# Performance work log

Hardware: AMD Instinct MI355X
Metric: run time of the kernel (lower is better)

The kernel has to match this reference:

```python
import jax, jax.numpy as jnp
import numpy as np

B, T, D = 4, 256, 512          # batch, seq_len, encoder_dim
L, H = 2, 8                    # num xLSTM blocks, num heads
I = 2 * D                      # inner dim (proj_factor=2)
DH = I // H                    # per-head dim = 128
K, G = 32, 64                  # mdn_components, goal_dim
EPS = 1e-5


def _ln(x, s, b):
    m = x.mean(-1, keepdims=True)
    v = jnp.mean((x - m) ** 2, -1, keepdims=True)
    return (x - m) * jax.lax.rsqrt(v + EPS) * s + b


def setup_inputs() -> dict:
    key = jax.random.key(0)
    ks = jax.random.split(key, 16)
    sc = 0.02
    nrm = lambda k, shp: jax.random.normal(k, shp, jnp.float32) * sc
    return {
        "x": jax.random.normal(ks[0], (B, T, D), jnp.float32),
        "ln_s": jnp.ones((L, D), jnp.float32),
        "ln_b": jnp.zeros((L, D), jnp.float32),
        "W_proj": nrm(ks[1], (L, D, 2 * I)),
        "Wq": nrm(ks[2], (L, I, I)),
        "Wk": nrm(ks[3], (L, I, I)),
        "Wv": nrm(ks[4], (L, I, I)),
        "Wi": nrm(ks[5], (L, I, H)),
        "bi": jnp.zeros((L, H), jnp.float32),
        "Wf": nrm(ks[6], (L, I, H)),
        "bf": jnp.full((L, H), 3.0, jnp.float32),  # forget-gate bias init
        "gn_s": jnp.ones((L, I), jnp.float32),
        "gn_b": jnp.zeros((L, I), jnp.float32),
        "W_down": nrm(ks[7], (L, I, D)),
        "fln_s": jnp.ones((D,), jnp.float32),
        "fln_b": jnp.zeros((D,), jnp.float32),
        "W_pi": nrm(ks[8], (D, K)),
        "b_pi": jnp.zeros((K,), jnp.float32),
        "W_mu": nrm(ks[9], (D, K * G)),
        "b_mu": jnp.zeros((K * G,), jnp.float32),
        "W_sig": nrm(ks[10], (D, K * G)),
        "b_sig": jnp.zeros((K * G,), jnp.float32),
    }


def _forward(x, ln_s, ln_b, W_proj, Wq, Wk, Wv, Wi, bi, Wf, bf,
             gn_s, gn_b, W_down, fln_s, fln_b,
             W_pi, b_pi, W_mu, b_mu, W_sig, b_sig):
    inv_sqrt_dh = 1.0 / (DH ** 0.5)

    def step(carry, x_t):  # x_t: (B, D); replicates per-timestep xlstm_stack.step()
        C, n, m = carry    # (L,B,H,DH,DH), (L,B,H,DH), (L,B,H)
        h = x_t
        for l in range(L):  # fixed small block loop
            skip = h
            xn = _ln(h, ln_s[l], ln_b[l])
            xp = xn @ W_proj[l]                      # (B, 2I)
            xm, z = jnp.split(xp, 2, axis=-1)        # mLSTM branch / gate branch
            q = (xm @ Wq[l]).reshape(B, H, DH)
            k = (xm @ Wk[l]).reshape(B, H, DH) * inv_sqrt_dh
            v = (xm @ Wv[l]).reshape(B, H, DH)
            ip = xm @ Wi[l] + bi[l]                  # (B, H) exp input gate preact
            fp = xm @ Wf[l] + bf[l]                  # (B, H) forget gate preact
            logf = jax.nn.log_sigmoid(fp)
            m_new = jnp.maximum(logf + m[l], ip)     # stabilizer
            ig = jnp.exp(ip - m_new)
            fg = jnp.exp(logf + m[l] - m_new)
            # matrix memory update: C <- f*C + i * k v^T ; n <- f*n + i*k
            C_new = fg[:, :, None, None] * C[l] + ig[:, :, None, None] * (k[..., :, None] * v[..., None, :])
            n_new = fg[..., None] * n[l] + ig[..., None] * k
            num = jnp.einsum('bhk,bhkv->bhv', q, C_new)
            den = jnp.maximum(jnp.abs(jnp.einsum('bhk,bhk->bh', q, n_new)), 1.0)
            hh = num / den[..., None]                # (B, H, DH)
            # multi-head norm (per-head layernorm, no per-head affine)
            mu_h = hh.mean(-1, keepdims=True)
            var_h = jnp.mean((hh - mu_h) ** 2, -1, keepdims=True)
            hh = (hh - mu_h) * jax.lax.rsqrt(var_h + EPS)
            hh = hh.reshape(B, I) * gn_s[l] + gn_b[l]
            hh = hh * jax.nn.silu(z)                 # output gating branch
            h = skip + hh @ W_down[l]                # residual
            C = C.at[l].set(C_new)
            n = n.at[l].set(n_new)
            m = m.at[l].set(m_new)
        return (C, n, m), h

    C0 = jnp.zeros((L, B, H, DH, DH), x.dtype)
    n0 = jnp.zeros((L, B, H, DH), x.dtype)
    m0 = jnp.zeros((L, B, H), x.dtype)
    _, hs = jax.lax.scan(step, (C0, n0, m0), jnp.swapaxes(x, 0, 1))
    last = _ln(hs[-1], fln_s, fln_b)                 # post-blocks norm on final step
    pi = jax.nn.softmax(last @ W_pi + b_pi, axis=-1)              # (B, K)
    mu = (last @ W_mu + b_mu).reshape(B, K, G)                     # (B, K, G)
    sigma = jax.nn.softplus(last @ W_sig + b_sig).reshape(B, K, G) # (B, K, G)
    return pi, mu, sigma


def reference(x, ln_s, ln_b, W_proj, Wq, Wk, Wv, Wi, bi, Wf, bf,
              gn_s, gn_b, W_down, fln_s, fln_b,
              W_pi, b_pi, W_mu, b_mu, W_sig, b_sig):
    return _forward(x, ln_s, ln_b, W_proj, Wq, Wk, Wv, Wi, bi, Wf, bf,
                    gn_s, gn_b, W_down, fln_s, fln_b,
                    W_pi, b_pi, W_mu, b_mu, W_sig, b_sig)
```

## Files before the change

kernel.cpp:

```cpp
#include <hip/hip_runtime.h>
#include <hip/hip_bf16.h>
#include <math.h>

#define DEV __device__ __forceinline__

typedef __attribute__((ext_vector_type(8))) short bf16x8;
typedef __attribute__((ext_vector_type(4))) float f32x4;

static DEV float softplus_f(float x){ return fmaxf(x,0.f) + log1pf(expf(-fabsf(x))); }
static DEV float logsig_f(float x){ return fminf(x,0.f) - log1pf(expf(-fabsf(x))); }
static DEV float silu_f(float x){ return x / (1.f + expf(-x)); }
static DEV unsigned short f2bf(float f){
  union { float f; unsigned u; } v; v.f = f;
  unsigned r = (v.u + 0x7fffu + ((v.u >> 16) & 1u)) >> 16;
  return (unsigned short)r;
}
static DEV float bf2f(unsigned short u){
  union { unsigned u; float f; } v; v.u = ((unsigned)u) << 16; return v.f;
}

__global__ void wconv_all(const float* __restrict__ Wp, const float* __restrict__ Wq,
                          const float* __restrict__ Wk, const float* __restrict__ Wv,
                          const float* __restrict__ Wd,
                          unsigned short* projT0, unsigned short* projT1,
                          unsigned short* qT0, unsigned short* kT0, unsigned short* kT1,
                          unsigned short* vT0, unsigned short* vT1, unsigned short* dT0)
{
  int z = blockIdx.z;
  const float* W; unsigned short* Wt; int K, M; float scale = 1.f;
  const float INV = 0.08838834764831845f;
  switch (z){
    case 0: W = Wp;              Wt = projT0; K = 512;  M = 2048; break;
    case 1: W = Wp + 512*2048;   Wt = projT1; K = 512;  M = 2048; break;
    case 2: W = Wq;              Wt = qT0;    K = 1024; M = 1024; break;
    case 3: W = Wk;              Wt = kT0;    K = 1024; M = 1024; scale = INV; break;
    case 4: W = Wk + 1048576;    Wt = kT1;    K = 1024; M = 1024; scale = INV; break;
    case 5: W = Wv;              Wt = vT0;    K = 1024; M = 1024; break;
    case 6: W = Wv + 1048576;    Wt = vT1;    K = 1024; M = 1024; break;
    default: W = Wd;             Wt = dT0;    K = 1024; M = 512;  break;
  }
  int m0 = blockIdx.x * 32, k0 = blockIdx.y * 32;
  if (m0 >= M || k0 >= K) return;
  __shared__ float s[32][33];
  int tx = threadIdx.x & 31, ty = threadIdx.x >> 5;
  #pragma unroll
  for (int u = 0; u < 32; u += 8)
    s[ty+u][tx] = W[(size_t)(k0+ty+u)*M + m0 + tx];
  __syncthreads();
  #pragma unroll
  for (int u = 0; u < 32; u += 8)
    Wt[(size_t)(m0+ty+u)*K + k0 + tx] = f2bf(s[tx][ty+u] * scale);
}

__global__ __launch_bounds__(256) void wcomb2(const float* __restrict__ W_proj,
                                              const float* __restrict__ Wi,
                                              const float* __restrict__ Wf,
                                              float* __restrict__ Wc)
{
  int gid = blockIdx.x * 4 + (threadIdx.x >> 6);
  int l = gid >> 9, d = gid & 511;
  int lane = threadIdx.x & 63;
  const float* wp = W_proj + (size_t)l*512*2048 + (size_t)d*2048 + lane*16;
  const float* wi = Wi + (size_t)l*1024*8;
  const float* wf = Wf + (size_t)l*1024*8;
  float acc[16];
  #pragma unroll
  for (int q = 0; q < 16; ++q) acc[q] = 0.f;
  #pragma unroll 4
  for (int u = 0; u < 16; ++u){
    float xv = wp[u];
    int j = lane*16 + u;
    float4 wi0 = *(const float4*)(wi + j*8);
    float4 wi1 = *(const float4*)(wi + j*8 + 4);
    float4 wf0 = *(const float4*)(wf + j*8);
    float4 wf1 = *(const float4*)(wf + j*8 + 4);
    acc[0]  = fmaf(xv, wi0.x, acc[0]);  acc[1]  = fmaf(xv, wi0.y, acc[1]);
    acc[2]  = fmaf(xv, wi0.z, acc[2]);  acc[3]  = fmaf(xv, wi0.w, acc[3]);
    acc[4]  = fmaf(xv, wi1.x, acc[4]);  acc[5]  = fmaf(xv, wi1.y, acc[5]);
    acc[6]  = fmaf(xv, wi1.z, acc[6]);  acc[7]  = fmaf(xv, wi1.w, acc[7]);
    acc[8]  = fmaf(xv, wf0.x, acc[8]);  acc[9]  = fmaf(xv, wf0.y, acc[9]);
    acc[10] = fmaf(xv, wf0.z, acc[10]); acc[11] = fmaf(xv, wf0.w, acc[11]);
    acc[12] = fmaf(xv, wf1.x, acc[12]); acc[13] = fmaf(xv, wf1.y, acc[13]);
    acc[14] = fmaf(xv, wf1.z, acc[14]); acc[15] = fmaf(xv, wf1.w, acc[15]);
  }
  #pragma unroll
  for (int o = 32; o > 0; o >>= 1){
    #pragma unroll
    for (int q = 0; q < 16; ++q) acc[q] += __shfl_xor(acc[q], o);
  }
  if (lane == 0){
    float* dst = Wc + (size_t)l*512*16 + d*16;
    #pragma unroll
    for (int q = 0; q < 16; ++q) dst[q] = acc[q];
  }
}

__global__ __launch_bounds__(256) void ln_gates(
    const float* __restrict__ in, unsigned short* __restrict__ outb,
    const float* __restrict__ s, const float* __restrict__ b,
    const float* __restrict__ Wc, float* __restrict__ ipfp)
{
  int r = blockIdx.x;
  const float* x = in + (size_t)r * 512;
  int tid = threadIdx.x;
  float lsum = 0.f, lsq = 0.f;
  for (int i = tid; i < 512; i += 256){ float v = x[i]; lsum += v; lsq += v*v; }
  #pragma unroll
  for (int o = 32; o > 0; o >>= 1){ lsum += __shfl_down(lsum, o); lsq += __shfl_down(lsq, o); }
  __shared__ float s1[4], s2[4];
  int wid = tid >> 6, lane = tid & 63;
  if (lane == 0){ s1[wid] = lsum; s2[wid] = lsq; }
  __syncthreads();
  if (tid == 0){ float a=0.f,c=0.f; for (int w=0; w<4; ++w){ a+=s1[w]; c+=s2[w]; } s1[0]=a; s2[0]=c; }
  __syncthreads();
  float mean = s1[0] * (1.f/512.f);
  float var  = s2[0] * (1.f/512.f) - mean*mean;
  float rstd = rsqrtf(var + 1e-5f);
  __shared__ float P[256][17];
  float g[16];
  #pragma unroll
  for (int q = 0; q < 16; ++q) g[q] = 0.f;
  for (int i = tid; i < 512; i += 256){
    float v = (x[i]-mean)*rstd*s[i] + b[i];
    outb[(size_t)r*512 + i] = f2bf(v);
    const float* wrow = Wc + i*16;
    #pragma unroll
    for (int q = 0; q < 16; ++q) g[q] = fmaf(v, wrow[q], g[q]);
  }
  #pragma unroll
  for (int q = 0; q < 16; ++q) P[tid][q] = g[q];
  __syncthreads();
  {
    int q = tid >> 4, c = tid & 15;
    float sacc = 0.f;
    #pragma unroll
    for (int u = 0; u < 16; ++u) sacc += P[c*16 + u][q];
    sacc += __shfl_xor(sacc, 1); sacc += __shfl_xor(sacc, 2);
    sacc += __shfl_xor(sacc, 4); sacc += __shfl_xor(sacc, 8);
    if (c == 0) ipfp[r*16 + q] = sacc;
  }
}

__global__ void ln_rows(const float* __restrict__ in, float* __restrict__ outf,
                        const float* __restrict__ s, const float* __restrict__ b, int D)
{
  int r = blockIdx.x;
  const float* x = in + (size_t)r * D;
  float lsum = 0.f, lsq = 0.f;
  for (int i = threadIdx.x; i < D; i += blockDim.x){ float v = x[i]; lsum += v; lsq += v*v; }
  #pragma unroll
  for (int o = 32; o > 0; o >>= 1){ lsum += __shfl_down(lsum, o); lsq += __shfl_down(lsq, o); }
  __shared__ float s1[4], s2[4];
  int wid = threadIdx.x >> 6, lane = threadIdx.x & 63;
  if (lane == 0){ s1[wid] = lsum; s2[wid] = lsq; }
  __syncthreads();
  if (threadIdx.x == 0){ float a=0.f,c=0.f; for (int w=0; w<4; ++w){ a+=s1[w]; c+=s2[w]; } s1[0]=a; s2[0]=c; }
  __syncthreads();
  float mean = s1[0] / D, var = s2[0] / D - mean*mean;
  float rstd = rsqrtf(var + 1e-5f);
  for (int i = threadIdx.x; i < D; i += blockDim.x)
    outf[(size_t)r*D + i] = (x[i]-mean)*rstd*s[i] + b[i];
}

__global__ __launch_bounds__(256) void gemm_mfma(
    const unsigned short* __restrict__ A, int lda,
    const unsigned short* __restrict__ Bt, int ldb,
    float* __restrict__ C, int ldc,
    unsigned short* __restrict__ Cbf,
    const float* __restrict__ skip, int ldskip,
    int K)
{
  __shared__ __align__(16) unsigned short As[64][72];
  __shared__ __align__(16) unsigned short Bs[64][72];
  int row0 = blockIdx.y * 64, col0 = blockIdx.x * 64;
  int tid = threadIdx.x;
  int w = tid >> 6, l = tid & 63;
  int wr = (w >> 1) * 32, wc = (w & 1) * 32;
  int lr = l & 15, lk = l >> 4;
  int r1 = tid >> 3, c1 = (tid & 7) * 8;
  int r2 = (tid + 256) >> 3, c2 = ((tid + 256) & 7) * 8;
  const unsigned short* a1 = A  + (size_t)(row0 + r1) * lda + c1;
  const unsigned short* a2 = A  + (size_t)(row0 + r2) * lda + c2;
  const unsigned short* b1 = Bt + (size_t)(col0 + r1) * ldb + c1;
  const unsigned short* b2 = Bt + (size_t)(col0 + r2) * ldb + c2;
  f32x4 acc00 = {0,0,0,0}, acc01 = {0,0,0,0}, acc10 = {0,0,0,0}, acc11 = {0,0,0,0};
  for (int k0 = 0; k0 < K; k0 += 64){
    *(bf16x8*)&As[r1][c1] = *(const bf16x8*)(a1 + k0);
    *(bf16x8*)&As[r2][c2] = *(const bf16x8*)(a2 + k0);
    *(bf16x8*)&Bs[r1][c1] = *(const bf16x8*)(b1 + k0);
    *(bf16x8*)&Bs[r2][c2] = *(const bf16x8*)(b2 + k0);
    __syncthreads();
    #pragma unroll
    for (int kk = 0; kk < 2; ++kk){
      bf16x8 a0 = *(const bf16x8*)&As[wr + lr][kk*32 + lk*8];
      bf16x8 a1f = *(const bf16x8*)&As[wr + 16 + lr][kk*32 + lk*8];
      bf16x8 b0 = *(const bf16x8*)&Bs[wc + lr][kk*32 + lk*8];
      bf16x8 b1f = *(const bf16x8*)&Bs[wc + 16 + lr][kk*32 + lk*8];
      acc00 = __builtin_amdgcn_mfma_f32_16x16x32_bf16(a0, b0, acc00, 0, 0, 0);
      acc01 = __builtin_amdgcn_mfma_f32_16x16x32_bf16(a0, b1f, acc01, 0, 0, 0);
      acc10 = __builtin_amdgcn_mfma_f32_16x16x32_bf16(a1f, b0, acc10, 0, 0, 0);
      acc11 = __builtin_amdgcn_mfma_f32_16x16x32_bf16(a1f, b1f, acc11, 0, 0, 0);
    }
    __syncthreads();
  }
  #pragma unroll
  for (int i = 0; i < 2; ++i){
    #pragma unroll
    for (int j = 0; j < 2; ++j){
      f32x4 a = (i == 0) ? ((j == 0) ? acc00 : acc01) : ((j == 0) ? acc10 : acc11);
      int col = col0 + wc + j*16 + lr;
      #pragma unroll
      for (int r = 0; r < 4; ++r){
        int row = row0 + wr + i*16 + lk*4 + r;
        float o = a[r];
        if (skip) o += skip[(size_t)row*ldskip + col];
        if (C)   C[(size_t)row*ldc + col] = o;
        if (Cbf) Cbf[(size_t)row*ldc + col] = f2bf(o);
      }
    }
  }
}

__global__ __launch_bounds__(256) void gemm_mfma_multi(
    const unsigned short* __restrict__ A, int lda,
    const unsigned short* __restrict__ Bt0, const unsigned short* __restrict__ Bt1,
    const unsigned short* __restrict__ Bt2, int ldb,
    unsigned short* __restrict__ C0, unsigned short* __restrict__ C1,
    unsigned short* __restrict__ C2, int ldc, int K)
{
  const unsigned short* Bt = (blockIdx.z == 0) ? Bt0 : (blockIdx.z == 1) ? Bt1 : Bt2;
  unsigned short* Cbf      = (blockIdx.z == 0) ? C0  : (blockIdx.z == 1) ? C1  : C2;
  __shared__ __align__(16) unsigned short As[64][72];
  __shared__ __align__(16) unsigned short Bs[64][72];
  int row0 = blockIdx.y * 64, col0 = blockIdx.x * 64;
  int tid = threadIdx.x;
  int w = tid >> 6, l = tid & 63;
  int wr = (w >> 1) * 32, wc = (w & 1) * 32;
  int lr = l & 15, lk = l >> 4;
  int r1 = tid >> 3, c1 = (tid & 7) * 8;
  int r2 = (tid + 256) >> 3, c2 = ((tid + 256) & 7) * 8;
  const unsigned short* a1 = A  + (size_t)(row0 + r1) * lda + c1;
  const unsigned short* a2 = A  + (size_t)(row0 + r2) * lda + c2;
  const unsigned short* b1 = Bt + (size_t)(col0 + r1) * ldb + c1;
  const unsigned short* b2 = Bt + (size_t)(col0 + r2) * ldb + c2;
  f32x4 acc00 = {0,0,0,0}, acc01 = {0,0,0,0}, acc10 = {0,0,0,0}, acc11 = {0,0,0,0};
  for (int k0 = 0; k0 < K; k0 += 64){
    *(bf16x8*)&As[r1][c1] = *(const bf16x8*)(a1 + k0);
    *(bf16x8*)&As[r2][c2] = *(const bf16x8*)(a2 + k0);
    *(bf16x8*)&Bs[r1][c1] = *(const bf16x8*)(b1 + k0);
    *(bf16x8*)&Bs[r2][c2] = *(const bf16x8*)(b2 + k0);
    __syncthreads();
    #pragma unroll
    for (int kk = 0; kk < 2; ++kk){
      bf16x8 a0 = *(const bf16x8*)&As[wr + lr][kk*32 + lk*8];
      bf16x8 a1f = *(const bf16x8*)&As[wr + 16 + lr][kk*32 + lk*8];
      bf16x8 b0 = *(const bf16x8*)&Bs[wc + lr][kk*32 + lk*8];
      bf16x8 b1f = *(const bf16x8*)&Bs[wc + 16 + lr][kk*32 + lk*8];
      acc00 = __builtin_amdgcn_mfma_f32_16x16x32_bf16(a0, b0, acc00, 0, 0, 0);
      acc01 = __builtin_amdgcn_mfma_f32_16x16x32_bf16(a0, b1f, acc01, 0, 0, 0);
      acc10 = __builtin_amdgcn_mfma_f32_16x16x32_bf16(a1f, b0, acc10, 0, 0, 0);
      acc11 = __builtin_amdgcn_mfma_f32_16x16x32_bf16(a1f, b1f, acc11, 0, 0, 0);
    }
    __syncthreads();
  }
  #pragma unroll
  for (int i = 0; i < 2; ++i){
    #pragma unroll
    for (int j = 0; j < 2; ++j){
      f32x4 a = (i == 0) ? ((j == 0) ? acc00 : acc01) : ((j == 0) ? acc10 : acc11);
      int col = col0 + wc + j*16 + lr;
      #pragma unroll
      for (int r = 0; r < 4; ++r){
        int row = row0 + wr + i*16 + lk*4 + r;
        Cbf[(size_t)row*ldc + col] = f2bf(a[r]);
      }
    }
  }
}

__global__ void scan_gates(const float* __restrict__ ipfp,
                           const float* __restrict__ bi, const float* __restrict__ bfg,
                           float* __restrict__ alpha, float* __restrict__ Mt)
{
  int bh = blockIdx.x; int b = bh >> 3, h = bh & 7;
  int lane = threadIdx.x;
  float bih = bi[h], bfh = bfg[h];
  float lf[4], ip[4];
  #pragma unroll
  for (int u = 0; u < 4; ++u){
    int t = lane*4 + u, r = b*256 + t;
    ip[u] = ipfp[r*16 + h] + bih;
    lf[u] = logsig_f(ipfp[r*16 + 8 + h] + bfh);
  }
  float c0 = lf[0], c1 = c0+lf[1], c2 = c1+lf[2], c3 = c2+lf[3];
  float tot = c3, pre = tot;
  #pragma unroll
  for (int o = 1; o < 64; o <<= 1){ float v = __shfl_up(pre, o); if (lane >= o) pre += v; }
  float excl = pre - tot;
  float F[4] = {excl+c0, excl+c1, excl+c2, excl+c3};
  float al[4];
  #pragma unroll
  for (int u = 0; u < 4; ++u) al[u] = ip[u] - F[u];
  float lm[4];
  lm[0] = al[0]; lm[1] = fmaxf(lm[0], al[1]); lm[2] = fmaxf(lm[1], al[2]); lm[3] = fmaxf(lm[2], al[3]);
  float pm = lm[3];
  #pragma unroll
  for (int o = 1; o < 64; o <<= 1){ float v = __shfl_up(pm, o); if (lane >= o) pm = fmaxf(pm, v); }
  float pmexcl = __shfl_up(pm, 1);
  if (lane == 0) pmexcl = -3.4e38f;
  int base = bh*256 + lane*4;
  #pragma unroll
  for (int u = 0; u < 4; ++u){
    alpha[base+u] = al[u];
    Mt[base+u] = fmaxf(0.f, fmaxf(pmexcl, lm[u]));
  }
}

__global__ __launch_bounds__(256) void attn_l0_mfma(
    const unsigned short* __restrict__ q, const unsigned short* __restrict__ k,
    const unsigned short* __restrict__ v,
    const float* __restrict__ alpha, const float* __restrict__ Mt,
    const unsigned short* __restrict__ xpb,
    const float* __restrict__ gn_s, const float* __restrict__ gn_b,
    unsigned short* __restrict__ gated)
{
  __shared__ __align__(16) char smem[46080];
  unsigned short (*Ks)[136] = (unsigned short(*)[136])smem;
  unsigned short (*Vt)[72]  = (unsigned short(*)[72])(smem + 17408);
  unsigned short (*Ps)[72]  = (unsigned short(*)[72])(smem + 35840);
  float* alpha_sh = (float*)(smem + 45056);
  float* Mt_sh    = (float*)(smem + 45312);
  float (*denL)[64] = (float(*)[64])(smem + 45568);
  float (*numf)[140] = (float(*)[140])smem;

  int blk = blockIdx.x;
  int tt = blk & 3, h = (blk >> 2) & 7, b = blk >> 5;
  int t0 = tt * 64;
  int tid = threadIdx.x;
  int w = tid >> 6, l = tid & 63;
  int wr = (w >> 1) * 32;
  int wc = (w & 1) * 32;
  int wd = (w & 1) * 64;
  int lrm = l & 15, lk = l >> 4;
  int bhT = ((b*8 + h) << 8);
  size_t headoff = (size_t)h * 128;

  {
    #pragma unroll
    for (int u = 0; u < 4; ++u){
      int o = u*256 + tid, row = o >> 4, oct = o & 15;
      *(bf16x8*)&Ks[row][oct*8] =
        *(const bf16x8*)(q + (size_t)(b*256 + t0 + row)*1024 + headoff + oct*8);
    }
    if (tid < 64) Mt_sh[tid] = Mt[bhT + t0 + tid];
    if (tid < 128) ((float*)denL)[tid] = 0.f;
  }
  __syncthreads();
  bf16x8 aq[2][4];
  #pragma unroll
  for (int i = 0; i < 2; ++i)
    #pragma unroll
    for (int kk = 0; kk < 4; ++kk)
      aq[i][kk] = *(const bf16x8*)&Ks[wr + i*16 + lrm][kk*32 + lk*8];
  __syncthreads();

  f32x4 pacc[2][4] = {};
  int ntile = tt + 1;

  for (int it = 0; it < ntile; ++it){
    int s0 = it * 64;
    #pragma unroll
    for (int u = 0; u < 4; ++u){
      int o = u*256 + tid, row = o >> 4, oct = o & 15;
      *(bf16x8*)&Ks[row][oct*8] =
        *(const bf16x8*)(k + (size_t)(b*256 + s0 + row)*1024 + headoff + oct*8);
    }
    #pragma unroll
    for (int u = 0; u < 2; ++u){
      int task = u*256 + tid;
      int sp = task & 31, oct = task >> 5;
      const unsigned short* vp = v + (size_t)(b*256 + s0 + sp*2)*1024 + headoff + oct*8;
      bf16x8 r0 = *(const bf16x8*)vp;
      bf16x8 r1 = *(const bf16x8*)(vp + 1024);
      #pragma unroll
      for (int j = 0; j < 8; ++j){
        unsigned lo = (unsigned short)r0[j];
        unsigned hi = (unsigned short)r1[j];
        *(unsigned*)&Vt[oct*8 + j][sp*2] = lo | (hi << 16);
      }
    }
    if (tid < 64) alpha_sh[tid] = alpha[bhT + s0 + tid];
    __syncthreads();

    f32x4 sacc[2][2] = {};
    #pragma unroll
    for (int kk = 0; kk < 4; ++kk){
      bf16x8 b0 = *(const bf16x8*)&Ks[wc + lrm][kk*32 + lk*8];
      bf16x8 b1 = *(const bf16x8*)&Ks[wc + 16 + lrm][kk*32 + lk*8];
      sacc[0][0] = __builtin_amdgcn_mfma_f32_16x16x32_bf16(aq[0][kk], b0, sacc[0][0], 0, 0, 0);
      sacc[0][1] = __builtin_amdgcn_mfma_f32_16x16x32_bf16(aq[0][kk], b1, sacc[0][1], 0, 0, 0);
      sacc[1][0] = __builtin_amdgcn_mfma_f32_16x16x32_bf16(aq[1][kk], b0, sacc[1][0], 0, 0, 0);
      sacc[1][1] = __builtin_amdgcn_mfma_f32_16x16x32_bf16(aq[1][kk], b1, sacc[1][1], 0, 0, 0);
    }

    bool diag = (it == ntile - 1);
    float av0 = alpha_sh[wc + lrm];
    float av1 = alpha_sh[wc + 16 + lrm];
    #pragma unroll
    for (int i = 0; i < 2; ++i){
      #pragma unroll
      for (int r = 0; r < 4; ++r){
        int tl = wr + i*16 + lk*4 + r;
        float mt = Mt_sh[tl];
        float p0 = __expf(av0 - mt) * sacc[i][0][r];
        float p1 = __expf(av1 - mt) * sacc[i][1][r];
        if (diag){
          if (wc + lrm      > tl) p0 = 0.f;
          if (wc + 16 + lrm > tl) p1 = 0.f;
        }
        Ps[tl][wc + lrm]      = f2bf(p0);
        Ps[tl][wc + 16 + lrm] = f2bf(p1);
        float dv = p0 + p1;
        dv += __shfl_xor(dv, 1); dv += __shfl_xor(dv, 2);
        dv += __shfl_xor(dv, 4); dv += __shfl_xor(dv, 8);
        if (lrm == 0) denL[w & 1][tl] += dv;
      }
    }
    __syncthreads();

    #pragma unroll
    for (int ks = 0; ks < 2; ++ks){
      bf16x8 pa0 = *(const bf16x8*)&Ps[wr + lrm][ks*32 + lk*8];
      bf16x8 pa1 = *(const bf16x8*)&Ps[wr + 16 + lrm][ks*32 + lk*8];
      #pragma unroll
      for (int jd = 0; jd < 4; ++jd){
        bf16x8 vb8 = *(const bf16x8*)&Vt[wd + jd*16 + lrm][ks*32 + lk*8];
        pacc[0][jd] = __builtin_amdgcn_mfma_f32_16x16x32_bf16(pa0, vb8, pacc[0][jd], 0, 0, 0);
        pacc[1][jd] = __builtin_amdgcn_mfma_f32_16x16x32_bf16(pa1, vb8, pacc[1][jd], 0, 0, 0);
      }
    }
    __syncthreads();
  }

  #pragma unroll
  for (int i = 0; i < 2; ++i)
    #pragma unroll
    for (int jd = 0; jd < 4; ++jd)
      #pragma unroll
      for (int r = 0; r < 4; ++r)
        numf[wr + i*16 + lk*4 + r][wd + jd*16 + lrm] = pacc[i][jd][r];
  if (tid < 64){
    float s = denL[0][tid] + denL[1][tid];
    alpha_sh[tid] = 1.0f / fmaxf(fabsf(s), 1.0f);
  }
  __syncthreads();

  {
    int row = tid >> 2, qq = tid & 3;
    float inv = alpha_sh[row];
    const float* nr = &numf[row][qq*32];
    float xs[32];
    float sum = 0.f, sq = 0.f;
    #pragma unroll
    for (int j = 0; j < 8; ++j){
      float4 t4 = *(const float4*)(nr + j*4);
      float v0 = t4.x*inv, v1 = t4.y*inv, v2 = t4.z*inv, v3 = t4.w*inv;
      xs[j*4+0] = v0; xs[j*4+1] = v1; xs[j*4+2] = v2; xs[j*4+3] = v3;
      sum += v0+v1+v2+v3;
      sq  += v0*v0+v1*v1+v2*v2+v3*v3;
    }
    sum += __shfl_xor(sum, 1); sq += __shfl_xor(sq, 1);
    sum += __shfl_xor(sum, 2); sq += __shfl_xor(sq, 2);
    float mean = sum * (1.f/128.f);
    float var  = sq  * (1.f/128.f) - mean*mean;
    float rstd = rsqrtf(var + 1e-5f);
    int rr = b*256 + t0 + row;
    const unsigned short* zp = xpb + (size_t)rr*2048 + 1024 + headoff + qq*32;
    const float* gsP = gn_s + headoff + qq*32;
    const float* gbP = gn_b + headoff + qq*32;
    unsigned short* op = gated + (size_t)rr*1024 + headoff + qq*32;
    #pragma unroll
    for (int j8 = 0; j8 < 4; ++j8){
      bf16x8 zv = *(const bf16x8*)(zp + j8*8);
      bf16x8 ov;
      #pragma unroll
      for (int j = 0; j < 8; ++j){
        int jj = j8*8 + j;
        float valn = (xs[jj]-mean)*rstd*gsP[jj] + gbP[jj];
        ov[j] = (short)f2bf(valn * silu_f(bf2f((unsigned short)zv[j])));
      }
      *(bf16x8*)(op + j8*8) = ov;
    }
  }
}

__global__ void qlast_split(const unsigned short* __restrict__ xpb, const float* __restrict__ Wq1,
                            float* __restrict__ part)
{
  int jt = blockIdx.x, ks = blockIdx.y;
  int j = jt*256 + threadIdx.x;
  __shared__ float xs[4][32];
  int t = threadIdx.x;
  if (t < 128){ int b = t >> 5, kk = t & 31; xs[b][kk] = bf2f(xpb[(size_t)(b*256+255)*2048 + ks*32 + kk]); }
  __syncthreads();
  float a0=0.f,a1=0.f,a2=0.f,a3=0.f;
  #pragma unroll 8
  for (int kk = 0; kk < 32; ++kk){
    float wv = Wq1[(size_t)(ks*32+kk)*1024 + j];
    a0 = fmaf(xs[0][kk], wv, a0);
    a1 = fmaf(xs[1][kk], wv, a1);
    a2 = fmaf(xs[2][kk], wv, a2);
    a3 = fmaf(xs[3][kk], wv, a3);
  }
  part[((size_t)ks*4 + 0)*1024 + j] = a0;
  part[((size_t)ks*4 + 1)*1024 + j] = a1;
  part[((size_t)ks*4 + 2)*1024 + j] = a2;
  part[((size_t)ks*4 + 3)*1024 + j] = a3;
}

__global__ void qlast_reduce(const float* __restrict__ part, float* __restrict__ q1last)
{
  int j = blockIdx.x*256 + threadIdx.x;
  float s = 0.f;
  for (int ks = 0; ks < 32; ++ks) s += part[(size_t)ks*4096 + j];
  q1last[j] = s;
}

__global__ __launch_bounds__(256) void attn_l1_split(
    const float* __restrict__ q1, const unsigned short* __restrict__ k1,
    const unsigned short* __restrict__ v1,
    const float* __restrict__ alpha, const float* __restrict__ Mt,
    float* __restrict__ pnum, float* __restrict__ pden)
{
  int sc = blockIdx.x, bh = blockIdx.y;
  int b = bh >> 3, h = bh & 7;
  int s0 = sc * 32;
  int tid = threadIdx.x;
  __shared__ float qsh[128];
  __shared__ float sred[32][9];
  __shared__ float as[32];
  __shared__ float nred[2][128];
  if (tid < 128) qsh[tid] = q1[b*1024 + h*128 + tid];
  __syncthreads();
  {
    int sl = tid & 31, dc = tid >> 5;
    const unsigned short* kp = k1 + (size_t)(b*256 + s0 + sl)*1024 + h*128 + dc*16;
    float p = 0.f;
    #pragma unroll
    for (int u = 0; u < 16; u += 8){
      bf16x8 kv = *(const bf16x8*)(kp + u);
      #pragma unroll
      for (int e = 0; e < 8; ++e) p = fmaf(qsh[dc*16+u+e], bf2f((unsigned short)kv[e]), p);
    }
    sred[sl][dc] = p;
  }
  __syncthreads();
  if (tid < 32){
    float sum = 0.f;
    #pragma unroll
    for (int dc = 0; dc < 8; ++dc) sum += sred[tid][dc];
    float w = __expf(alpha[bh*256 + s0 + tid] - Mt[bh*256 + 255]);
    as[tid] = w * sum;
  }
  __syncthreads();
  {
    int d = tid & 127, sg = tid >> 7;
    const unsigned short* vp = v1 + (size_t)(b*256 + s0 + sg*16)*1024 + h*128 + d;
    float np = 0.f;
    #pragma unroll
    for (int u = 0; u < 16; ++u) np = fmaf(as[sg*16 + u], bf2f(vp[(size_t)u*1024]), np);
    nred[sg][d] = np;
  }
  __syncthreads();
  if (tid < 128) pnum[((size_t)bh*8 + sc)*128 + tid] = nred[0][tid] + nred[1][tid];
  if (tid == 128){
    float dsum = 0.f;
    #pragma unroll
    for (int u = 0; u < 32; ++u) dsum += as[u];
    pden[bh*8 + sc] = dsum;
  }
}

__global__ __launch_bounds__(128) void attn_l1_fin(
    const float* __restrict__ pnum, const float* __restrict__ pden,
    const unsigned short* __restrict__ xpb,
    const float* __restrict__ gn_s, const float* __restrict__ gn_b,
    float* __restrict__ gated1)
{
  int bh = blockIdx.x; int b = bh >> 3, h = bh & 7;
  int tid = threadIdx.x;
  __shared__ float hh[128];
  __shared__ float dsh, msh, rsh;
  float nsum = 0.f;
  #pragma unroll
  for (int sc = 0; sc < 8; ++sc) nsum += pnum[((size_t)bh*8 + sc)*128 + tid];
  if (tid == 0){
    float d = 0.f;
    #pragma unroll
    for (int sc = 0; sc < 8; ++sc) d += pden[bh*8 + sc];
    dsh = fmaxf(fabsf(d), 1.0f);
  }
  __syncthreads();
  float hv = nsum / dsh;
  hh[tid] = hv;
  __syncthreads();
  if (tid < 64){
    float a = hh[tid], c = hh[tid + 64];
    float s1 = a + c, s2v = a*a + c*c;
    #pragma unroll
    for (int o = 32; o > 0; o >>= 1){ s1 += __shfl_down(s1, o); s2v += __shfl_down(s2v, o); }
    if (tid == 0){
      float mean = s1*(1.f/128.f);
      float var  = s2v*(1.f/128.f) - mean*mean;
      msh = mean; rsh = rsqrtf(var + 1e-5f);
    }
  }
  __syncthreads();
  {
    int i = h*128 + tid;
    float valn = (hv - msh)*rsh*gn_s[i] + gn_b[i];
    float z = bf2f(xpb[(size_t)(b*256 + 255)*2048 + 1024 + i]);
    gated1[b*1024 + i] = valn * silu_f(z);
  }
}

__global__ void dl_split(const float* __restrict__ gated1, const float* __restrict__ Wd,
                         float* __restrict__ part)
{
  int jt = blockIdx.x, ks = blockIdx.y;
  int j = jt*256 + threadIdx.x;
  __shared__ float xs[4][32];
  int t = threadIdx.x;
  if (t < 128){ int b = t >> 5, kk = t & 31; xs[b][kk] = gated1[b*1024 + ks*32 + kk]; }
  __syncthreads();
  float a0=0.f,a1=0.f,a2=0.f,a3=0.f;
  #pragma unroll 8
  for (int kk = 0; kk < 32; ++kk){
    float wv = Wd[(size_t)(ks*32+kk)*512 + j];
    a0 = fmaf(xs[0][kk], wv, a0);
    a1 = fmaf(xs[1][kk], wv, a1);
    a2 = fmaf(xs[2][kk], wv, a2);
    a3 = fmaf(xs[3][kk], wv, a3);
  }
  part[((size_t)ks*4 + 0)*512 + j] = a0;
  part[((size_t)ks*4 + 1)*512 + j] = a1;
  part[((size_t)ks*4 + 2)*512 + j] = a2;
  part[((size_t)ks*4 + 3)*512 + j] = a3;
}

__global__ void dl_reduce(const float* __restrict__ part, const float* __restrict__ h0,
                          float* __restrict__ hfinal)
{
  int j2 = blockIdx.x*256 + threadIdx.x;
  int b = j2 >> 9, jj = j2 & 511;
  float s = 0.f;
  for (int ks = 0; ks < 32; ++ks) s += part[((size_t)ks*4 + b)*512 + jj];
  hfinal[j2] = h0[(size_t)(b*256 + 255)*512 + jj] + s;
}

__global__ void ms_split(const float* __restrict__ last,
                         const float* __restrict__ W_mu, const float* __restrict__ W_sig,
                         float* __restrict__ part)
{
  int jt = blockIdx.x, ks = blockIdx.y, mat = blockIdx.z;
  int j = jt*256 + threadIdx.x;
  const float* W = mat ? W_sig : W_mu;
  __shared__ float xs[4][64];
  int t = threadIdx.x;
  { int b = t >> 6, kk = t & 63; xs[b][kk] = last[b*512 + ks*64 + kk]; }
  __syncthreads();
  float a0=0.f,a1=0.f,a2=0.f,a3=0.f;
  #pragma unroll 8
  for (int kk = 0; kk < 64; ++kk){
    float wv = W[(size_t)(ks*64+kk)*2048 + j];
    a0 = fmaf(xs[0][kk], wv, a0);
    a1 = fmaf(xs[1][kk], wv, a1);
    a2 = fmaf(xs[2][kk], wv, a2);
    a3 = fmaf(xs[3][kk], wv, a3);
  }
  size_t base = ((size_t)(mat*8 + ks)*4);
  part[(base + 0)*2048 + j] = a0;
  part[(base + 1)*2048 + j] = a1;
  part[(base + 2)*2048 + j] = a2;
  part[(base + 3)*2048 + j] = a3;
}

__global__ void ms_reduce(const float* __restrict__ part,
                          const float* __restrict__ b_mu, const float* __restrict__ b_sig,
                          float* __restrict__ out)
{
  int j = blockIdx.x*256 + threadIdx.x;
  int b = blockIdx.y, mat = blockIdx.z;
  float s = mat ? b_sig[j] : b_mu[j];
  for (int ks = 0; ks < 8; ++ks) s += part[((size_t)(mat*8 + ks)*4 + b)*2048 + j];
  out[128 + mat*8192 + b*2048 + j] = mat ? softplus_f(s) : s;
}

__global__ void heads_pi(const float* __restrict__ last,
                         const float* __restrict__ W_pi, const float* __restrict__ b_pi,
                         float* __restrict__ out)
{
  __shared__ float ls[512];
  int b = blockIdx.x, o = threadIdx.x;
  for (int i = o; i < 512; i += 64) ls[i] = last[b*512 + i];
  __syncthreads();
  bool valid = o < 32;
  float acc = -3.4e38f;
  if (valid){
    acc = b_pi[o];
    for (int i = 0; i < 512; ++i) acc = fmaf(ls[i], W_pi[i*32 + o], acc);
  }
  float m = acc;
  #pragma unroll
  for (int o2 = 32; o2 > 0; o2 >>= 1) m = fmaxf(m, __shfl_xor(m, o2));
  float e = valid ? expf(acc - m) : 0.f;
  float ssum = e;
  #pragma unroll
  for (int o2 = 32; o2 > 0; o2 >>= 1) ssum += __shfl_xor(ssum, o2);
  if (valid) out[b*32 + o] = e / ssum;
}

extern "C" void kernel_launch(void* const* d_in, const int* in_sizes, int n_in,
                              void* d_out, int out_size, void* d_ws, size_t ws_size,
                              hipStream_t stream)
{
  const float* x      = (const float*)d_in[0];
  const float* ln_s   = (const float*)d_in[1];
  const float* ln_b   = (const float*)d_in[2];
  const float* W_proj = (const float*)d_in[3];
  const float* Wq     = (const float*)d_in[4];
  const float* Wk     = (const float*)d_in[5];
  const float* Wv     = (const float*)d_in[6];
  const float* Wi     = (const float*)d_in[7];
  const float* bi     = (const float*)d_in[8];
  const float* Wf     = (const float*)d_in[9];
  const float* bf     = (const float*)d_in[10];
  const float* gn_s   = (const float*)d_in[11];
  const float* gn_b   = (const float*)d_in[12];
  const float* W_down = (const float*)d_in[13];
  const float* fln_s  = (const float*)d_in[14];
  const float* fln_b  = (const float*)d_in[15];
  const float* W_pi   = (const float*)d_in[16];
  const float* b_pi   = (const float*)d_in[17];
  const float* W_mu   = (const float*)d_in[18];
  const float* b_mu   = (const float*)d_in[19];
  const float* W_sig  = (const float*)d_in[20];
  const float* b_sig  = (const float*)d_in[21];
  float* out = (float*)d_out;

  char* p = (char*)d_ws;
  unsigned short* projT0 = (unsigned short*)p; p += (size_t)2048*512*2;
  unsigned short* projT1 = (unsigned short*)p; p += (size_t)2048*512*2;
  unsigned short* qT0    = (unsigned short*)p; p += (size_t)1024*1024*2;
  unsigned short* kT0    = (unsigned short*)p; p += (size_t)1024*1024*2;
  unsigned short* kT1    = (unsigned short*)p; p += (size_t)1024*1024*2;
  unsigned short* vT0    = (unsigned short*)p; p += (size_t)1024*1024*2;
  unsigned short* vT1    = (unsigned short*)p; p += (size_t)1024*1024*2;
  unsigned short* dT0    = (unsigned short*)p; p += (size_t)512*1024*2;
  float* Wc              = (float*)p;          p += (size_t)2*512*16*4;
  unsigned short* xnb    = (unsigned short*)p; p += (size_t)1024*512*2;
  unsigned short* xpb    = (unsigned short*)p; p += (size_t)1024*2048*2;
  unsigned short* qbb    = (unsigned short*)p; p += (size_t)1024*1024*2;
  unsigned short* kbb    = (unsigned short*)p; p += (size_t)1024*1024*2;
  unsigned short* vbb    = (unsigned short*)p; p += (size_t)1024*1024*2;
  unsigned short* gatedb = (unsigned short*)p; p += (size_t)1024*1024*2;
  float* h0     = (float*)p; p += (size_t)1024*512*4;
  float* ipfp   = (float*)p; p += (size_t)16384*4;
  float* alpha  = (float*)p; p += (size_t)8192*4;
  float* Mtb    = (float*)p; p += (size_t)8192*4;
  float* q1last = (float*)p; p += (size_t)4096*4;
  float* gated1 = (float*)p; p += (size_t)4096*4;
  float* hfinal = (float*)p; p += (size_t)2048*4;
  float* lastb  = (float*)p; p += (size_t)2048*4;
  float* qpart  = (float*)p; p += (size_t)32*4096*4;
  float* dpart  = (float*)p; p += (size_t)32*4*512*4;
  float* pnum   = (float*)p; p += (size_t)32*8*128*4;
  float* pden   = (float*)p; p += (size_t)32*8*4;
  float* mspart = (float*)p; p += (size_t)16*4*2048*4;

  const float* ln_s1 = ln_s + 512;
  const float* ln_b1 = ln_b + 512;
  const float* gn_s1 = gn_s + 1024;
  const float* gn_b1 = gn_b + 1024;
  const float* Wq1   = Wq + 1024*1024;
  const float* Wd1   = W_down + 1024*512;

  dim3 blk256(256);

  wconv_all<<<dim3(64,32,8), blk256, 0, stream>>>(W_proj, Wq, Wk, Wv, W_down,
      projT0, projT1, qT0, kT0, kT1, vT0, vT1, dT0);
  wcomb2<<<256, blk256, 0, stream>>>(W_proj, Wi, Wf, Wc);

  ln_gates<<<1024, blk256, 0, stream>>>(x, xnb, ln_s, ln_b, Wc, ipfp);
  gemm_mfma<<<dim3(32,16), blk256, 0, stream>>>(xnb, 512, projT0, 512, nullptr, 2048, xpb, nullptr, 0, 512);
  gemm_mfma_multi<<<dim3(16,16,3), blk256, 0, stream>>>(xpb, 2048, qT0, kT0, vT0, 1024, qbb, kbb, vbb, 1024, 1024);
  scan_gates<<<32, 64, 0, stream>>>(ipfp, bi, bf, alpha, Mtb);
  attn_l0_mfma<<<128, blk256, 0, stream>>>(qbb, kbb, vbb, alpha, Mtb, xpb, gn_s, gn_b, gatedb);
  gemm_mfma<<<dim3(8,16), blk256, 0, stream>>>(gatedb, 1024, dT0, 1024, h0, 512, nullptr, x, 512, 1024);

  ln_gates<<<1024, blk256, 0, stream>>>(h0, xnb, ln_s1, ln_b1, Wc + 512*16, ipfp);
  gemm_mfma<<<dim3(32,16), blk256, 0, stream>>>(xnb, 512, projT1, 512, nullptr, 2048, xpb, nullptr, 0, 512);
  gemm_mfma_multi<<<dim3(16,16,2), blk256, 0, stream>>>(xpb, 2048, kT1, vT1, vT1, 1024, kbb, vbb, vbb, 1024, 1024);
  scan_gates<<<32, 64, 0, stream>>>(ipfp, bi + 8, bf + 8, alpha, Mtb);
  qlast_split<<<dim3(4,32), blk256, 0, stream>>>(xpb, Wq1, qpart);
  qlast_reduce<<<16, blk256, 0, stream>>>(qpart, q1last);
  attn_l1_split<<<dim3(8,32), blk256, 0, stream>>>(q1last, kbb, vbb, alpha, Mtb, pnum, pden);
  attn_l1_fin<<<32, 128, 0, stream>>>(pnum, pden, xpb, gn_s1, gn_b1, gated1);
  dl_split<<<dim3(2,32), blk256, 0, stream>>>(gated1, Wd1, dpart);
  dl_reduce<<<8, blk256, 0, stream>>>(dpart, h0, hfinal);

  ln_rows<<<4, blk256, 0, stream>>>(hfinal, lastb, fln_s, fln_b, 512);
  ms_split<<<dim3(8,8,2), blk256, 0, stream>>>(lastb, W_mu, W_sig, mspart);
  ms_reduce<<<dim3(8,4,2), blk256, 0, stream>>>(mspart, b_mu, b_sig, out);
  heads_pi<<<4, 64, 0, stream>>>(lastb, W_pi, b_pi, out);
}
```

Measured before the change: 215.6 us.

## Use 128x128 MFMA GEMM tiles and fold small reduce kernels into consumers

Replaces the 64x64-tile projection and QKV GEMMs with a 128x128-tile MFMA kernel where each wave computes a 4x4 grid of 16x16 fragments, so each shared-memory load feeds more MFMAs. The qlast_reduce kernel is removed and its partial-sum reduction moves into attn_l1_split. dl_reduce and ln_rows are merged into a single dl_fin kernel. These cut launch count and redundant global round trips. The larger tiles launch far fewer blocks (128 or 192 per GEMM), which may underfill the GPU's CUs, and they raise register pressure.

```diff
diff --git a/kernel.cpp b/kernel.cpp
--- a/kernel.cpp
+++ b/kernel.cpp
@@ -141,25 +141,58 @@
   }
 }
 
-__global__ void ln_rows(const float* __restrict__ in, float* __restrict__ outf,
-                        const float* __restrict__ s, const float* __restrict__ b, int D)
-{
-  int r = blockIdx.x;
-  const float* x = in + (size_t)r * D;
-  float lsum = 0.f, lsq = 0.f;
-  for (int i = threadIdx.x; i < D; i += blockDim.x){ float v = x[i]; lsum += v; lsq += v*v; }
-  #pragma unroll
-  for (int o = 32; o > 0; o >>= 1){ lsum += __shfl_down(lsum, o); lsq += __shfl_down(lsq, o); }
-  __shared__ float s1[4], s2[4];
-  int wid = threadIdx.x >> 6, lane = threadIdx.x & 63;
-  if (lane == 0){ s1[wid] = lsum; s2[wid] = lsq; }
-  __syncthreads();
-  if (threadIdx.x == 0){ float a=0.f,c=0.f; for (int w=0; w<4; ++w){ a+=s1[w]; c+=s2[w]; } s1[0]=a; s2[0]=c; }
-  __syncthreads();
-  float mean = s1[0] / D, var = s2[0] / D - mean*mean;
-  float rstd = rsqrtf(var + 1e-5f);
-  for (int i = threadIdx.x; i < D; i += blockDim.x)
-    outf[(size_t)r*D + i] = (x[i]-mean)*rstd*s[i] + b[i];
+__global__ __launch_bounds__(256) void gemm_mfma128_multi(
+    const unsigned short* __restrict__ A, int lda,
+    const unsigned short* __restrict__ Bt0, const unsigned short* __restrict__ Bt1,
+    const unsigned short* __restrict__ Bt2, int ldb,
+    unsigned short* __restrict__ C0, unsigned short* __restrict__ C1,
+    unsigned short* __restrict__ C2, int ldc, int K)
+{
+  const unsigned short* Bt = (blockIdx.z == 0) ? Bt0 : (blockIdx.z == 1) ? Bt1 : Bt2;
+  unsigned short* Cbf      = (blockIdx.z == 0) ? C0  : (blockIdx.z == 1) ? C1  : C2;
+  __shared__ __align__(16) unsigned short As[128][72];
+  __shared__ __align__(16) unsigned short Bs[128][72];
+  int row0 = blockIdx.y * 128, col0 = blockIdx.x * 128;
+  int tid = threadIdx.x;
+  int w = tid >> 6, l = tid & 63;
+  int wr = (w >> 1) * 64, wc = (w & 1) * 64;
+  int lr = l & 15, lk = l >> 4;
+  f32x4 acc[4][4] = {};
+  for (int k0 = 0; k0 < K; k0 += 64){
+    #pragma unroll
+    for (int u = 0; u < 4; ++u){
+      int o = u*256 + tid, r = o >> 3, c = (o & 7) * 8;
+      *(bf16x8*)&As[r][c] = *(const bf16x8*)(A  + (size_t)(row0 + r) * lda + k0 + c);
+      *(bf16x8*)&Bs[r][c] = *(const bf16x8*)(Bt + (size_t)(col0 + r) * ldb + k0 + c);
+    }
+    __syncthreads();
+    #pragma unroll
+    for (int kk = 0; kk < 2; ++kk){
+      bf16x8 af[4], bfr[4];
+      #pragma unroll
+      for (int i = 0; i < 4; ++i) af[i]  = *(const bf16x8*)&As[wr + i*16 + lr][kk*32 + lk*8];
+      #pragma unroll
+      for (int j = 0; j < 4; ++j) bfr[j] = *(const bf16x8*)&Bs[wc + j*16 + lr][kk*32 + lk*8];
+      #pragma unroll
+      for (int i = 0; i < 4; ++i)
+        #pragma unroll
+        for (int j = 0; j < 4; ++j)
+          acc[i][j] = __builtin_amdgcn_mfma_f32_16x16x32_bf16(af[i], bfr[j], acc[i][j], 0, 0, 0);
+    }
+    __syncthreads();
+  }
+  #pragma unroll
+  for (int i = 0; i < 4; ++i){
+    #pragma unroll
+    for (int j = 0; j < 4; ++j){
+      int col = col0 + wc + j*16 + lr;
+      #pragma unroll
+      for (int r = 0; r < 4; ++r){
+        int row = row0 + wr + i*16 + lk*4 + r;
+        Cbf[(size_t)row*ldc + col] = f2bf(acc[i][j][r]);
+      }
+    }
+  }
 }
 
 __global__ __launch_bounds__(256) void gemm_mfma(
@@ -221,63 +254,6 @@
   }
 }
 
-__global__ __launch_bounds__(256) void gemm_mfma_multi(
-    const unsigned short* __restrict__ A, int lda,
-    const unsigned short* __restrict__ Bt0, const unsigned short* __restrict__ Bt1,
-    const unsigned short* __restrict__ Bt2, int ldb,
-    unsigned short* __restrict__ C0, unsigned short* __restrict__ C1,
-    unsigned short* __restrict__ C2, int ldc, int K)
-{
-  const unsigned short* Bt = (blockIdx.z == 0) ? Bt0 : (blockIdx.z == 1) ? Bt1 : Bt2;
-  unsigned short* Cbf      = (blockIdx.z == 0) ? C0  : (blockIdx.z == 1) ? C1  : C2;
-  __shared__ __align__(16) unsigned short As[64][72];
-  __shared__ __align__(16) unsigned short Bs[64][72];
-  int row0 = blockIdx.y * 64, col0 = blockIdx.x * 64;
-  int tid = threadIdx.x;
-  int w = tid >> 6, l = tid & 63;
-  int wr = (w >> 1) * 32, wc = (w & 1) * 32;
-  int lr = l & 15, lk = l >> 4;
-  int r1 = tid >> 3, c1 = (tid & 7) * 8;
-  int r2 = (tid + 256) >> 3, c2 = ((tid + 256) & 7) * 8;
-  const unsigned short* a1 = A  + (size_t)(row0 + r1) * lda + c1;
-  const unsigned short* a2 = A  + (size_t)(row0 + r2) * lda + c2;
-  const unsigned short* b1 = Bt + (size_t)(col0 + r1) * ldb + c1;
-  const unsigned short* b2 = Bt + (size_t)(col0 + r2) * ldb + c2;
-  f32x4 acc00 = {0,0,0,0}, acc01 = {0,0,0,0}, acc10 = {0,0,0,0}, acc11 = {0,0,0,0};
-  for (int k0 = 0; k0 < K; k0 += 64){
-    *(bf16x8*)&As[r1][c1] = *(const bf16x8*)(a1 + k0);
-    *(bf16x8*)&As[r2][c2] = *(const bf16x8*)(a2 + k0);
-    *(bf16x8*)&Bs[r1][c1] = *(const bf16x8*)(b1 + k0);
-    *(bf16x8*)&Bs[r2][c2] = *(const bf16x8*)(b2 + k0);
-    __syncthreads();
-    #pragma unroll
-    for (int kk = 0; kk < 2; ++kk){
-      bf16x8 a0 = *(const bf16x8*)&As[wr + lr][kk*32 + lk*8];
-      bf16x8 a1f = *(const bf16x8*)&As[wr + 16 + lr][kk*32 + lk*8];
-      bf16x8 b0 = *(const bf16x8*)&Bs[wc + lr][kk*32 + lk*8];
-      bf16x8 b1f = *(const bf16x8*)&Bs[wc + 16 + lr][kk*32 + lk*8];
-      acc00 = __builtin_amdgcn_mfma_f32_16x16x32_bf16(a0, b0, acc00, 0, 0, 0);
-      acc01 = __builtin_amdgcn_mfma_f32_16x16x32_bf16(a0, b1f, acc01, 0, 0, 0);
-      acc10 = __builtin_amdgcn_mfma_f32_16x16x32_bf16(a1f, b0, acc10, 0, 0, 0);
-      acc11 = __builtin_amdgcn_mfma_f32_16x16x32_bf16(a1f, b1f, acc11, 0, 0, 0);
-    }
-    __syncthreads();
-  }
-  #pragma unroll
-  for (int i = 0; i < 2; ++i){
-    #pragma unroll
-    for (int j = 0; j < 2; ++j){
-      f32x4 a = (i == 0) ? ((j == 0) ? acc00 : acc01) : ((j == 0) ? acc10 : acc11);
-      int col = col0 + wc + j*16 + lr;
-      #pragma unroll
-      for (int r = 0; r < 4; ++r){
-        int row = row0 + wr + i*16 + lk*4 + r;
-        Cbf[(size_t)row*ldc + col] = f2bf(a[r]);
-      }
-    }
-  }
-}
-
 __global__ void scan_gates(const float* __restrict__ ipfp,
                            const float* __restrict__ bi, const float* __restrict__ bfg,
                            float* __restrict__ alpha, float* __restrict__ Mt)
@@ -518,16 +494,8 @@
   part[((size_t)ks*4 + 3)*1024 + j] = a3;
 }
 
-__global__ void qlast_reduce(const float* __restrict__ part, float* __restrict__ q1last)
-{
-  int j = blockIdx.x*256 + threadIdx.x;
-  float s = 0.f;
-  for (int ks = 0; ks < 32; ++ks) s += part[(size_t)ks*4096 + j];
-  q1last[j] = s;
-}
-
 __global__ __launch_bounds__(256) void attn_l1_split(
-    const float* __restrict__ q1, const unsigned short* __restrict__ k1,
+    const float* __restrict__ qpart, const unsigned short* __restrict__ k1,
     const unsigned short* __restrict__ v1,
     const float* __restrict__ alpha, const float* __restrict__ Mt,
     float* __restrict__ pnum, float* __restrict__ pden)
@@ -540,7 +508,12 @@
   __shared__ float sred[32][9];
   __shared__ float as[32];
   __shared__ float nred[2][128];
-  if (tid < 128) qsh[tid] = q1[b*1024 + h*128 + tid];
+  if (tid < 128){
+    float s = 0.f;
+    #pragma unroll 8
+    for (int ks = 0; ks < 32; ++ks) s += qpart[((size_t)ks*4 + b)*1024 + h*128 + tid];
+    qsh[tid] = s;
+  }
   __syncthreads();
   {
     int sl = tid & 31, dc = tid >> 5;
@@ -648,14 +621,39 @@
   part[((size_t)ks*4 + 3)*512 + j] = a3;
 }
 
-__global__ void dl_reduce(const float* __restrict__ part, const float* __restrict__ h0,
-                          float* __restrict__ hfinal)
-{
-  int j2 = blockIdx.x*256 + threadIdx.x;
-  int b = j2 >> 9, jj = j2 & 511;
-  float s = 0.f;
-  for (int ks = 0; ks < 32; ++ks) s += part[((size_t)ks*4 + b)*512 + jj];
-  hfinal[j2] = h0[(size_t)(b*256 + 255)*512 + jj] + s;
+__global__ __launch_bounds__(256) void dl_fin(
+    const float* __restrict__ part, const float* __restrict__ h0,
+    const float* __restrict__ fln_s, const float* __restrict__ fln_b,
+    float* __restrict__ lastb)
+{
+  int b = blockIdx.x;
+  int tid = threadIdx.x;
+  float v[2];
+  #pragma unroll
+  for (int u = 0; u < 2; ++u){
+    int jj = tid*2 + u;
+    float s = 0.f;
+    #pragma unroll 8
+    for (int ks = 0; ks < 32; ++ks) s += part[((size_t)ks*4 + b)*512 + jj];
+    v[u] = h0[(size_t)(b*256 + 255)*512 + jj] + s;
+  }
+  float lsum = v[0] + v[1], lsq = v[0]*v[0] + v[1]*v[1];
+  #pragma unroll
+  for (int o = 32; o > 0; o >>= 1){ lsum += __shfl_down(lsum, o); lsq += __shfl_down(lsq, o); }
+  __shared__ float s1[4], s2[4];
+  int wid = tid >> 6, lane = tid & 63;
+  if (lane == 0){ s1[wid] = lsum; s2[wid] = lsq; }
+  __syncthreads();
+  if (tid == 0){ float a=0.f,c=0.f; for (int w2=0; w2<4; ++w2){ a+=s1[w2]; c+=s2[w2]; } s1[0]=a; s2[0]=c; }
+  __syncthreads();
+  float mean = s1[0] * (1.f/512.f);
+  float var  = s2[0] * (1.f/512.f) - mean*mean;
+  float rstd = rsqrtf(var + 1e-5f);
+  #pragma unroll
+  for (int u = 0; u < 2; ++u){
+    int jj = tid*2 + u;
+    lastb[b*512 + jj] = (v[u]-mean)*rstd*fln_s[jj] + fln_b[jj];
+  }
 }
 
 __global__ void ms_split(const float* __restrict__ last,
@@ -768,9 +766,7 @@
   float* ipfp   = (float*)p; p += (size_t)16384*4;
   float* alpha  = (float*)p; p += (size_t)8192*4;
   float* Mtb    = (float*)p; p += (size_t)8192*4;
-  float* q1last = (float*)p; p += (size_t)4096*4;
   float* gated1 = (float*)p; p += (size_t)4096*4;
-  float* hfinal = (float*)p; p += (size_t)2048*4;
   float* lastb  = (float*)p; p += (size_t)2048*4;
   float* qpart  = (float*)p; p += (size_t)32*4096*4;
   float* dpart  = (float*)p; p += (size_t)32*4*512*4;
@@ -792,24 +788,22 @@
   wcomb2<<<256, blk256, 0, stream>>>(W_proj, Wi, Wf, Wc);
 
   ln_gates<<<1024, blk256, 0, stream>>>(x, xnb, ln_s, ln_b, Wc, ipfp);
-  gemm_mfma<<<dim3(32,16), blk256, 0, stream>>>(xnb, 512, projT0, 512, nullptr, 2048, xpb, nullptr, 0, 512);
-  gemm_mfma_multi<<<dim3(16,16,3), blk256, 0, stream>>>(xpb, 2048, qT0, kT0, vT0, 1024, qbb, kbb, vbb, 1024, 1024);
+  gemm_mfma128_multi<<<dim3(16,8,1), blk256, 0, stream>>>(xnb, 512, projT0, projT0, projT0, 512, xpb, xpb, xpb, 2048, 512);
+  gemm_mfma128_multi<<<dim3(8,8,3), blk256, 0, stream>>>(xpb, 2048, qT0, kT0, vT0, 1024, qbb, kbb, vbb, 1024, 1024);
   scan_gates<<<32, 64, 0, stream>>>(ipfp, bi, bf, alpha, Mtb);
   attn_l0_mfma<<<128, blk256, 0, stream>>>(qbb, kbb, vbb, alpha, Mtb, xpb, gn_s, gn_b, gatedb);
   gemm_mfma<<<dim3(8,16), blk256, 0, stream>>>(gatedb, 1024, dT0, 1024, h0, 512, nullptr, x, 512, 1024);
 
   ln_gates<<<1024, blk256, 0, stream>>>(h0, xnb, ln_s1, ln_b1, Wc + 512*16, ipfp);
-  gemm_mfma<<<dim3(32,16), blk256, 0, stream>>>(xnb, 512, projT1, 512, nullptr, 2048, xpb, nullptr, 0, 512);
-  gemm_mfma_multi<<<dim3(16,16,2), blk256, 0, stream>>>(xpb, 2048, kT1, vT1, vT1, 1024, kbb, vbb, vbb, 1024, 1024);
+  gemm_mfma128_multi<<<dim3(16,8,1), blk256, 0, stream>>>(xnb, 512, projT1, projT1, projT1, 512, xpb, xpb, xpb, 2048, 512);
+  gemm_mfma128_multi<<<dim3(8,8,2), blk256, 0, stream>>>(xpb, 2048, kT1, vT1, vT1, 1024, kbb, vbb, vbb, 1024, 1024);
   scan_gates<<<32, 64, 0, stream>>>(ipfp, bi + 8, bf + 8, alpha, Mtb);
   qlast_split<<<dim3(4,32), blk256, 0, stream>>>(xpb, Wq1, qpart);
-  qlast_reduce<<<16, blk256, 0, stream>>>(qpart, q1last);
-  attn_l1_split<<<dim3(8,32), blk256, 0, stream>>>(q1last, kbb, vbb, alpha, Mtb, pnum, pden);
+  attn_l1_split<<<dim3(8,32), blk256, 0, stream>>>(qpart, kbb, vbb, alpha, Mtb, pnum, pden);
   attn_l1_fin<<<32, 128, 0, stream>>>(pnum, pden, xpb, gn_s1, gn_b1, gated1);
   dl_split<<<dim3(2,32), blk256, 0, stream>>>(gated1, Wd1, dpart);
-  dl_reduce<<<8, blk256, 0, stream>>>(dpart, h0, hfinal);
-
-  ln_rows<<<4, blk256, 0, stream>>>(hfinal, lastb, fln_s, fln_b, 512);
+  dl_fin<<<4, blk256, 0, stream>>>(dpart, h0, fln_s, fln_b, lastb);
+
   ms_split<<<dim3(8,8,2), blk256, 0, stream>>>(lastb, W_mu, W_sig, mspart);
   ms_reduce<<<dim3(8,4,2), blk256, 0, stream>>>(mspart, b_mu, b_sig, out);
   heads_pi<<<4, 64, 0, stream>>>(lastb, W_pi, b_pi, out);
```

Measured after the change: 197.2 us. -8.6%, faster.
